# Optimization experiments

Measured on AMD Instinct MI355X. Metric: run time of the kernel, lower is better.

## Reference

```python
import jax, jax.numpy as jnp
import numpy as np

N = 50000      # nodes
E = 800000     # edges
NIN = 512      # input features
NHID = 128     # hidden
NCLS = 64      # classes


def setup_inputs() -> dict:
    key = jax.random.key(0)
    k0, k1, k2, k3 = jax.random.split(key, 4)
    x = jax.random.normal(k0, (N, NIN), dtype=jnp.float32)
    edge_index = jax.random.randint(k1, (2, E), 0, N, dtype=jnp.int64)
    # Glorot-style init for GCNConv linear weights (bias starts at zero in PyG)
    W1 = jax.random.normal(k2, (NIN, NHID), dtype=jnp.float32) * (1.0 / np.sqrt(NIN))
    W2 = jax.random.normal(k3, (NHID, NCLS), dtype=jnp.float32) * (1.0 / np.sqrt(NHID))
    b1 = jnp.zeros((NHID,), dtype=jnp.float32)
    b2 = jnp.zeros((NCLS,), dtype=jnp.float32)
    return {"x": x, "edge_index": edge_index, "W1": W1, "b1": b1, "W2": W2, "b2": b2}


def gcn_conv(x, W, b, src, dst, n):
    """PyG GCNConv: linear transform, then sym-normalized aggregation with self-loops."""
    xw = x @ W                                                  # [n, out]
    ones = jnp.ones(src.shape[0], dtype=xw.dtype)
    deg = jax.ops.segment_sum(ones, dst, num_segments=n) + 1.0  # +1 for self-loop
    dinv = jax.lax.rsqrt(deg)                                   # deg >= 1
    norm = dinv[src] * dinv[dst]                                # [E]
    agg = jax.ops.segment_sum(xw[src] * norm[:, None], dst, num_segments=n)
    agg = agg + (dinv * dinv)[:, None] * xw                     # self-loop messages
    return agg + b


def reference(x, edge_index, W1, b1, W2, b2):
    src, dst = edge_index[0], edge_index[1]
    n = x.shape[0]
    # eval mode: dropout is a no-op; bn is defined but unused in forward
    h = gcn_conv(x, W1, b1, src, dst, n)
    h = jax.nn.relu(h)
    o = gcn_conv(h, W2, b2, src, dst, n)
    return jax.nn.log_softmax(o, axis=1)
```

## Files before the change

kernel.cpp:

```cpp
#include <hip/hip_runtime.h>
#include <hip/hip_bf16.h>
#include <cstdint>
#include <cstddef>

#define NNODES 50000
#define NEDGES 800000
#define NIN    512
#define NHID   128
#define NCLS   64

#define SCAN_BLK 512
#define SCAN_NB ((NNODES + SCAN_BLK - 1) / SCAN_BLK)

typedef __attribute__((ext_vector_type(8))) short bf16x8;
typedef __attribute__((ext_vector_type(4))) float f32x4;

static __device__ __forceinline__ ushort f2bf(float f) {
    uint32_t u = __float_as_uint(f);
    uint32_t r = (u + 0x7fffu + ((u >> 16) & 1u)) >> 16;
    return (ushort)r;
}
static __device__ __forceinline__ float bf2f(ushort b) {
    return __uint_as_float(((uint32_t)b) << 16);
}


__global__ void deg_kernel(const int* __restrict__ dst, int* __restrict__ deg) {
    int e = blockIdx.x * blockDim.x + threadIdx.x;
    if (e < NEDGES) atomicAdd(&deg[dst[e]], 1);
}

__global__ __launch_bounds__(SCAN_BLK) void scan1_kernel(const int* __restrict__ deg,
                                                         int* __restrict__ blkSum,
                                                         float* __restrict__ dinv) {
    int i = blockIdx.x * SCAN_BLK + threadIdx.x;
    int d = (i < NNODES) ? deg[i] : 0;
    if (i < NNODES) dinv[i] = rsqrtf((float)d + 1.0f);
    int v = d;
#pragma unroll
    for (int off = 32; off; off >>= 1) v += __shfl_xor(v, off, 64);
    __shared__ int ws[SCAN_BLK / 64];
    int w = threadIdx.x >> 6;
    if ((threadIdx.x & 63) == 0) ws[w] = v;
    __syncthreads();
    if (threadIdx.x == 0) {
        int s = 0;
#pragma unroll
        for (int k = 0; k < SCAN_BLK / 64; ++k) s += ws[k];
        blkSum[blockIdx.x] = s;
    }
}

__global__ void scan2_kernel(int* __restrict__ blkSum, int* __restrict__ rowptr) {
    __shared__ int sh[128];
    int t = threadIdx.x;
    int v = (t < SCAN_NB) ? blkSum[t] : 0;
    sh[t] = v;
    __syncthreads();
    for (int off = 1; off < 128; off <<= 1) {
        int o = (t >= off) ? sh[t - off] : 0;
        __syncthreads();
        sh[t] += o;
        __syncthreads();
    }
    if (t < SCAN_NB) blkSum[t] = sh[t] - v;
    if (t == 0) rowptr[NNODES] = NEDGES;
}

__global__ __launch_bounds__(SCAN_BLK) void scan3_kernel(const int* __restrict__ deg,
                                                         const int* __restrict__ blkOff,
                                                         int* __restrict__ rowptr) {
    int i = blockIdx.x * SCAN_BLK + threadIdx.x;
    int v = (i < NNODES) ? deg[i] : 0;
    int lane = threadIdx.x & 63;
    int w = threadIdx.x >> 6;
    int inc = v;
#pragma unroll
    for (int off = 1; off < 64; off <<= 1) {
        int o = __shfl_up(inc, off, 64);
        if (lane >= off) inc += o;
    }
    __shared__ int ws[SCAN_BLK / 64];
    if (lane == 63) ws[w] = inc;
    __syncthreads();
    int wpre = 0;
    for (int k = 0; k < w; ++k) wpre += ws[k];
    if (i < NNODES) rowptr[i] = inc - v + wpre + blkOff[blockIdx.x];
}

__global__ void scatter_kernel(const int* __restrict__ src, const int* __restrict__ dst,
                               const int* __restrict__ rowptr, int* __restrict__ cursor,
                               const float* __restrict__ dinv, int2* __restrict__ csr) {
    int e = blockIdx.x * blockDim.x + threadIdx.x;
    if (e >= NEDGES) return;
    int d = dst[e];
    int s = src[e];
    int pos = rowptr[d] + atomicAdd(&cursor[d], 1);
    csr[pos] = make_int2(s, __float_as_int(dinv[s]));
}

template <int NOUT, int KS, int CF>
__global__ void pack_kernel(const float* __restrict__ W, ushort* __restrict__ pack) {
    int t = blockIdx.x * blockDim.x + threadIdx.x;
    if (t >= KS * CF * 64 * 8) return;
    int j = t & 7;
    int lane = (t >> 3) & 63;
    int cf = (t >> 9) % CF;
    int ks = t / (CF * 512);
    int k = ks * 32 + (lane >> 4) * 8 + j;
    int c = cf * 16 + (lane & 15);
    pack[t] = f2bf(W[(size_t)k * NOUT + c]);
}

__global__ __launch_bounds__(256) void gemm1_kernel(const float* __restrict__ A,
                                                    const ushort* __restrict__ packB,
                                                    ushort* __restrict__ C) {
    int wid = (blockIdx.x * blockDim.x + threadIdx.x) >> 6;
    int lane = threadIdx.x & 63;
    int rowBase = wid * 16;
    if (rowBase >= NNODES) return;
    int rl = lane & 15;
    int kg = lane >> 4;
    const float* ap = A + (size_t)(rowBase + rl) * NIN + kg * 8;
    const ushort* bp = packB + (size_t)lane * 8;

    f32x4 acc[8];
#pragma unroll
    for (int cf = 0; cf < 8; ++cf) acc[cf] = (f32x4)(0.f);

    float4 a0[4], a1[4];
    bf16x8 bb[2][8];
#pragma unroll
    for (int p = 0; p < 3; ++p) {
        a0[p] = *(const float4*)(ap + p * 32);
        a1[p] = *(const float4*)(ap + p * 32 + 4);
    }
#pragma unroll
    for (int cf = 0; cf < 8; ++cf) bb[0][cf] = *(const bf16x8*)(bp + cf * 512);

#pragma unroll
    for (int ks = 0; ks < 16; ++ks) {
        if (ks + 3 < 16) {
            a0[(ks + 3) & 3] = *(const float4*)(ap + (ks + 3) * 32);
            a1[(ks + 3) & 3] = *(const float4*)(ap + (ks + 3) * 32 + 4);
        }
        if (ks + 1 < 16) {
#pragma unroll
            for (int cf = 0; cf < 8; ++cf)
                bb[(ks + 1) & 1][cf] = *(const bf16x8*)(bp + (ks + 1) * 4096 + cf * 512);
        }
        float4 x0 = a0[ks & 3], x1 = a1[ks & 3];
        bf16x8 af;
        af[0] = (short)f2bf(x0.x); af[1] = (short)f2bf(x0.y);
        af[2] = (short)f2bf(x0.z); af[3] = (short)f2bf(x0.w);
        af[4] = (short)f2bf(x1.x); af[5] = (short)f2bf(x1.y);
        af[6] = (short)f2bf(x1.z); af[7] = (short)f2bf(x1.w);
#pragma unroll
        for (int cf = 0; cf < 8; ++cf)
            acc[cf] = __builtin_amdgcn_mfma_f32_16x16x32_bf16(af, bb[ks & 1][cf], acc[cf], 0, 0, 0);
    }
#pragma unroll
    for (int cf = 0; cf < 8; ++cf)
#pragma unroll
        for (int j = 0; j < 4; ++j)
            C[(size_t)(rowBase + kg * 4 + j) * NHID + cf * 16 + rl] = f2bf(acc[cf][j]);
}

__global__ __launch_bounds__(256) void gemm2_kernel(const ushort* __restrict__ A,
                                                    const ushort* __restrict__ packB,
                                                    ushort* __restrict__ C) {
    int wid = (blockIdx.x * blockDim.x + threadIdx.x) >> 6;
    int lane = threadIdx.x & 63;
    int rowBase = wid * 16;
    if (rowBase >= NNODES) return;
    int rl = lane & 15;
    int kg = lane >> 4;
    const ushort* ap = A + (size_t)(rowBase + rl) * NHID + kg * 8;

    f32x4 acc[4];
#pragma unroll
    for (int cf = 0; cf < 4; ++cf) acc[cf] = (f32x4)(0.f);

#pragma unroll
    for (int ks = 0; ks < 4; ++ks) {
        bf16x8 af = *(const bf16x8*)(ap + ks * 32);
        const ushort* bp = packB + ((size_t)(ks * 4) * 64 + lane) * 8;
#pragma unroll
        for (int cf = 0; cf < 4; ++cf) {
            bf16x8 bf = *(const bf16x8*)(bp + (size_t)cf * 512);
            acc[cf] = __builtin_amdgcn_mfma_f32_16x16x32_bf16(af, bf, acc[cf], 0, 0, 0);
        }
    }
#pragma unroll
    for (int cf = 0; cf < 4; ++cf)
#pragma unroll
        for (int j = 0; j < 4; ++j)
            C[(size_t)(rowBase + kg * 4 + j) * NCLS + cf * 16 + rl] = f2bf(acc[cf][j]);
}

__global__ __launch_bounds__(256) void agg1_kernel(const ushort* __restrict__ xw,
                                                   const int* __restrict__ rowptr,
                                                   const int2* __restrict__ csr,
                                                   const float* __restrict__ dinv,
                                                   const float* __restrict__ b1,
                                                   ushort* __restrict__ h) {
    int wid = (blockIdx.x * blockDim.x + threadIdx.x) >> 6;
    int lane = threadIdx.x & 63;
    if (wid >= NNODES) return;
    int beg = rowptr[wid], end = rowptr[wid + 1];
    float a0 = 0.f, a1 = 0.f;
    int j = beg;
    for (; j + 8 <= end; j += 8) {
        int2 e[8];
#pragma unroll
        for (int q = 0; q < 8; ++q) e[q] = csr[j + q];
        uint v[8];
#pragma unroll
        for (int q = 0; q < 8; ++q) v[q] = *(const uint*)&xw[(size_t)e[q].x * NHID + lane * 2];
#pragma unroll
        for (int q = 0; q < 8; ++q) {
            float wq = __int_as_float(e[q].y);
            a0 += wq * __uint_as_float(v[q] << 16);
            a1 += wq * __uint_as_float(v[q] & 0xffff0000u);
        }
    }
    for (; j < end; ++j) {
        int2 e = csr[j];
        float w = __int_as_float(e.y);
        uint v = *(const uint*)&xw[(size_t)e.x * NHID + lane * 2];
        a0 += w * __uint_as_float(v << 16);
        a1 += w * __uint_as_float(v & 0xffff0000u);
    }
    float di = dinv[wid];
    float sl = di * di;
    uint xv = *(const uint*)&xw[(size_t)wid * NHID + lane * 2];
    float2 bv = *(const float2*)&b1[lane * 2];
    float r0 = di * a0 + sl * __uint_as_float(xv << 16) + bv.x;
    float r1 = di * a1 + sl * __uint_as_float(xv & 0xffff0000u) + bv.y;
    uint o = (uint)f2bf(fmaxf(r0, 0.f)) | ((uint)f2bf(fmaxf(r1, 0.f)) << 16);
    *(uint*)&h[(size_t)wid * NHID + lane * 2] = o;
}

__global__ __launch_bounds__(256) void agg2_kernel(const ushort* __restrict__ xw,
                                                   const int* __restrict__ rowptr,
                                                   const int2* __restrict__ csr,
                                                   const float* __restrict__ dinv,
                                                   const float* __restrict__ b2,
                                                   float* __restrict__ out) {
    int wid = (blockIdx.x * blockDim.x + threadIdx.x) >> 6;
    int lane = threadIdx.x & 63;
    if (wid >= NNODES) return;
    int beg = rowptr[wid], end = rowptr[wid + 1];
    float a = 0.f;
    int j = beg;
    for (; j + 8 <= end; j += 8) {
        int2 e[8];
#pragma unroll
        for (int q = 0; q < 8; ++q) e[q] = csr[j + q];
        float v[8];
#pragma unroll
        for (int q = 0; q < 8; ++q) v[q] = bf2f(xw[(size_t)e[q].x * NCLS + lane]);
#pragma unroll
        for (int q = 0; q < 8; ++q) a += __int_as_float(e[q].y) * v[q];
    }
    for (; j < end; ++j) {
        int2 e = csr[j];
        a += __int_as_float(e.y) * bf2f(xw[(size_t)e.x * NCLS + lane]);
    }
    float di = dinv[wid];
    float o = di * a + di * di * bf2f(xw[(size_t)wid * NCLS + lane]) + b2[lane];
    float m = o;
#pragma unroll
    for (int off = 32; off; off >>= 1) m = fmaxf(m, __shfl_xor(m, off, 64));
    float ex = __expf(o - m);
    float ssum = ex;
#pragma unroll
    for (int off = 32; off; off >>= 1) ssum += __shfl_xor(ssum, off, 64);
    out[(size_t)wid * NCLS + lane] = (o - m) - __logf(ssum);
}


extern "C" void kernel_launch(void* const* d_in, const int* in_sizes, int n_in,
                              void* d_out, int out_size, void* d_ws, size_t ws_size,
                              hipStream_t stream) {
    const float* x  = (const float*)d_in[0];
    const int*   ei = (const int*)d_in[1];
    const int*   src = ei;
    const int*   dst = ei + NEDGES;
    const float* W1 = (const float*)d_in[2];
    const float* b1 = (const float*)d_in[3];
    const float* W2 = (const float*)d_in[4];
    const float* b2 = (const float*)d_in[5];
    float* out = (float*)d_out;

    char* w = (char*)d_ws;
    auto alloc = [&](size_t bytes) {
        char* p = w;
        w += (bytes + 255) & ~(size_t)255;
        return p;
    };
    int*    deg    = (int*)alloc((size_t)2 * NNODES * 4);
    int*    cursor = deg + NNODES;
    int*    rowptr = (int*)alloc((NNODES + 1) * 4);
    int*    blkSum = (int*)alloc(SCAN_NB * 4);
    int2*   csr    = (int2*)alloc((size_t)NEDGES * 8);
    float*  dinv   = (float*)alloc(NNODES * 4);
    ushort* pack1  = (ushort*)alloc((size_t)16 * 8 * 64 * 8 * 2);
    ushort* pack2  = (ushort*)alloc((size_t)4 * 4 * 64 * 8 * 2);
    ushort* xw1    = (ushort*)alloc((size_t)NNODES * NHID * 2);
    ushort* h      = (ushort*)alloc((size_t)NNODES * NHID * 2);
    ushort* xw2    = (ushort*)alloc((size_t)NNODES * NCLS * 2);

    hipMemsetAsync(deg, 0, (size_t)2 * NNODES * 4, stream);

    deg_kernel<<<(NEDGES + 255) / 256, 256, 0, stream>>>(dst, deg);
    scan1_kernel<<<SCAN_NB, SCAN_BLK, 0, stream>>>(deg, blkSum, dinv);
    scan2_kernel<<<1, 128, 0, stream>>>(blkSum, rowptr);
    scan3_kernel<<<SCAN_NB, SCAN_BLK, 0, stream>>>(deg, blkSum, rowptr);
    scatter_kernel<<<(NEDGES + 255) / 256, 256, 0, stream>>>(src, dst, rowptr, cursor, dinv, csr);

    pack_kernel<NHID, 16, 8><<<(16 * 8 * 64 * 8 + 255) / 256, 256, 0, stream>>>(W1, pack1);
    pack_kernel<NCLS, 4, 4><<<(4 * 4 * 64 * 8 + 255) / 256, 256, 0, stream>>>(W2, pack2);

    gemm1_kernel<<<(NNODES / 16 + 3) / 4, 256, 0, stream>>>(x, pack1, xw1);
    agg1_kernel<<<(NNODES * 64 + 255) / 256, 256, 0, stream>>>(xw1, rowptr, csr, dinv, b1, h);

    gemm2_kernel<<<(NNODES / 16 + 3) / 4, 256, 0, stream>>>(h, pack2, xw2);
    agg2_kernel<<<(NNODES * 64 + 255) / 256, 256, 0, stream>>>(xw2, rowptr, csr, dinv, b2, out);
}
```

Before: 217.8 us.

## Stage gemm1 A tiles into LDS via async global_load_lds double buffering

Rewrites the first GEMM to stream 64-row by 64-float chunks of the fp32 input into double-buffered, XOR-swizzled shared memory using direct global-to-LDS loads. Each block now covers 64 rows with four waves, and the main loop is restructured around chunked stages. Register prefetch of A and B is removed, and B fragments are read directly from global each step. The aim is better coalescing and overlap of the dominant input read, at the cost of LDS usage and barriers.

```diff
diff --git a/kernel.cpp b/kernel.cpp
--- a/kernel.cpp
+++ b/kernel.cpp
@@ -115,55 +115,68 @@
 __global__ __launch_bounds__(256) void gemm1_kernel(const float* __restrict__ A,
                                                     const ushort* __restrict__ packB,
                                                     ushort* __restrict__ C) {
-    int wid = (blockIdx.x * blockDim.x + threadIdx.x) >> 6;
-    int lane = threadIdx.x & 63;
-    int rowBase = wid * 16;
-    if (rowBase >= NNODES) return;
-    int rl = lane & 15;
-    int kg = lane >> 4;
-    const float* ap = A + (size_t)(rowBase + rl) * NIN + kg * 8;
-    const ushort* bp = packB + (size_t)lane * 8;
+    __shared__ float lds[2][64 * 64];
+    const int t = threadIdx.x;
+    const int lane = t & 63;
+    const int w = t >> 6;
+    const int rowBase = blockIdx.x * 64;
+    const int rl = lane & 15;
+    const int kg = lane >> 4;
+
+    const int Rloc = (w << 2) + (lane >> 4);
+    const int csw = ((lane & 15) << 4) ^ ((Rloc & 7) << 4);
+    const char* Abase = (const char*)A;
+
+    const int xr = (rl & 7) << 4;
 
     f32x4 acc[8];
 #pragma unroll
     for (int cf = 0; cf < 8; ++cf) acc[cf] = (f32x4)(0.f);
 
-    float4 a0[4], a1[4];
-    bf16x8 bb[2][8];
-#pragma unroll
-    for (int p = 0; p < 3; ++p) {
-        a0[p] = *(const float4*)(ap + p * 32);
-        a1[p] = *(const float4*)(ap + p * 32 + 4);
-    }
-#pragma unroll
-    for (int cf = 0; cf < 8; ++cf) bb[0][cf] = *(const bf16x8*)(bp + cf * 512);
-
-#pragma unroll
-    for (int ks = 0; ks < 16; ++ks) {
-        if (ks + 3 < 16) {
-            a0[(ks + 3) & 3] = *(const float4*)(ap + (ks + 3) * 32);
-            a1[(ks + 3) & 3] = *(const float4*)(ap + (ks + 3) * 32 + 4);
-        }
-        if (ks + 1 < 16) {
-#pragma unroll
-            for (int cf = 0; cf < 8; ++cf)
-                bb[(ks + 1) & 1][cf] = *(const bf16x8*)(bp + (ks + 1) * 4096 + cf * 512);
-        }
-        float4 x0 = a0[ks & 3], x1 = a1[ks & 3];
-        bf16x8 af;
-        af[0] = (short)f2bf(x0.x); af[1] = (short)f2bf(x0.y);
-        af[2] = (short)f2bf(x0.z); af[3] = (short)f2bf(x0.w);
-        af[4] = (short)f2bf(x1.x); af[5] = (short)f2bf(x1.y);
-        af[6] = (short)f2bf(x1.z); af[7] = (short)f2bf(x1.w);
-#pragma unroll
-        for (int cf = 0; cf < 8; ++cf)
-            acc[cf] = __builtin_amdgcn_mfma_f32_16x16x32_bf16(af, bb[ks & 1][cf], acc[cf], 0, 0, 0);
-    }
+    auto stage = [&](int buf, int chunk) {
+#pragma unroll
+        for (int r = 0; r < 4; ++r) {
+            int row = rowBase + r * 16 + Rloc;
+            if (row > NNODES - 1) row = NNODES - 1;
+            const char* src = Abase + (size_t)row * (NIN * 4) + chunk * 256 + csw;
+            char* dst = (char*)&lds[buf][0] + r * 4096 + w * 1024 + lane * 16;
+            __builtin_amdgcn_global_load_lds((const uint32_t*)src, (uint32_t*)dst, 16, 0, 0);
+        }
+    };
+
+    stage(0, 0);
+    int buf = 0;
+#pragma unroll
+    for (int tch = 0; tch < 8; ++tch) {
+        __syncthreads();
+        if (tch + 1 < 8) stage(buf ^ 1, tch + 1);
+        const char* lrow = (const char*)&lds[buf][0] + (w * 16 + rl) * 256;
+#pragma unroll
+        for (int ks = 0; ks < 2; ++ks) {
+            float4 x0 = *(const float4*)(lrow + ((ks * 128 + kg * 32) ^ xr));
+            float4 x1 = *(const float4*)(lrow + ((ks * 128 + kg * 32 + 16) ^ xr));
+            bf16x8 af;
+            af[0] = (short)f2bf(x0.x); af[1] = (short)f2bf(x0.y);
+            af[2] = (short)f2bf(x0.z); af[3] = (short)f2bf(x0.w);
+            af[4] = (short)f2bf(x1.x); af[5] = (short)f2bf(x1.y);
+            af[6] = (short)f2bf(x1.z); af[7] = (short)f2bf(x1.w);
+            const ushort* bpp = packB + ((size_t)(tch * 2 + ks) * 8) * 512 + (size_t)lane * 8;
+#pragma unroll
+            for (int cf = 0; cf < 8; ++cf) {
+                bf16x8 bfv = *(const bf16x8*)(bpp + cf * 512);
+                acc[cf] = __builtin_amdgcn_mfma_f32_16x16x32_bf16(af, bfv, acc[cf], 0, 0, 0);
+            }
+        }
+        buf ^= 1;
+    }
+    const int rowW = rowBase + w * 16;
 #pragma unroll
     for (int cf = 0; cf < 8; ++cf)
 #pragma unroll
-        for (int j = 0; j < 4; ++j)
-            C[(size_t)(rowBase + kg * 4 + j) * NHID + cf * 16 + rl] = f2bf(acc[cf][j]);
+        for (int j = 0; j < 4; ++j) {
+            int rr = rowW + kg * 4 + j;
+            if (rr < NNODES) C[(size_t)rr * NHID + cf * 16 + rl] = f2bf(acc[cf][j]);
+        }
 }
 
 __global__ __launch_bounds__(256) void gemm2_kernel(const ushort* __restrict__ A,
@@ -322,7 +335,7 @@
     pack_kernel<NHID, 16, 8><<<(16 * 8 * 64 * 8 + 255) / 256, 256, 0, stream>>>(W1, pack1);
     pack_kernel<NCLS, 4, 4><<<(4 * 4 * 64 * 8 + 255) / 256, 256, 0, stream>>>(W2, pack2);
 
-    gemm1_kernel<<<(NNODES / 16 + 3) / 4, 256, 0, stream>>>(x, pack1, xw1);
+    gemm1_kernel<<<(NNODES + 63) / 64, 256, 0, stream>>>(x, pack1, xw1);
     agg1_kernel<<<(NNODES * 64 + 255) / 256, 256, 0, stream>>>(xw1, rowptr, csr, dinv, b1, h);
 
     gemm2_kernel<<<(NNODES / 16 + 3) / 4, 256, 0, stream>>>(h, pack2, xw2);
```

Measured after the change: 212.7 us. 1.02x faster.
